# Kernel optimization log

Measured on AMD Instinct MI355X. Metric: run time of the kernel, lower is better.

Reference implementation:

```python
import jax, jax.numpy as jnp
import numpy as np
from jax import lax

HID = 768          # hidden_dim / embedding_dim
IN = 64            # input_dim = max_seq_length // num_heads
SEQ = 512          # max_seq_length
GROUPS = IN        # conv groups
BLUR_K = 5
BLUR_SIGMA = 1.0


def _gauss1d(k, sigma):
    half = (k - 1) * 0.5
    x = np.linspace(-half, half, k)
    pdf = np.exp(-0.5 * (x / sigma) ** 2)
    return pdf / pdf.sum()


def setup_inputs() -> dict:
    key = jax.random.key(0)
    ks = jax.random.split(key, 8)
    s = 0.02
    return {
        "inputs": jax.random.normal(ks[0], (16, SEQ, HID), jnp.float32),
        # Conv1d(768, 768, k=3, groups=64): weight [out_ch, in_ch/groups, k]
        "conv_w": jax.random.normal(ks[1], (HID, HID // GROUPS, 3), jnp.float32) * s,
        "conv_b": jnp.zeros((HID,), jnp.float32),
        "ln_g": jnp.ones((IN,), jnp.float32),
        "ln_b": jnp.zeros((IN,), jnp.float32),
        # function_info: Linear(64, 64), torch weight convention [out, in]
        "fi_w": jax.random.normal(ks[2], (IN, IN), jnp.float32) * s,
        "fi_b": jnp.zeros((IN,), jnp.float32),
        # block_info: Linear(64, 1)
        "bi_w": jax.random.normal(ks[3], (1, IN), jnp.float32) * s,
        "bi_b": jnp.zeros((1,), jnp.float32),
    }


def _forward(inputs, conv_w, conv_b, ln_g, ln_b, fi_w, fi_b, bi_w, bi_b):
    x = inputs.reshape(-1, HID, IN)  # [Bn, 768, 64] (raw row-major view, as torch .view)
    q = k = v = m = x

    # q: grouped Conv1d + residual, GELU, LayerNorm over last dim (64)
    qc = lax.conv_general_dilated(
        q, conv_w, window_strides=(1,), padding=[(1, 1)],
        feature_group_count=GROUPS, dimension_numbers=("NCH", "OIH", "NCH"))
    qc = qc + conv_b[None, :, None]
    q = jax.nn.gelu(qc + q, approximate=False)
    mu = jnp.mean(q, axis=-1, keepdims=True)
    var = jnp.mean(jnp.square(q - mu), axis=-1, keepdims=True)
    q = (q - mu) * lax.rsqrt(var + 1e-5) * ln_g + ln_b

    # v: Linear(64,64) + GELU
    v = jax.nn.gelu(v @ fi_w.T + fi_b, approximate=False)

    # k: dropout (eval -> identity), softmax over dim=-2 (channel axis), GELU
    k = jax.nn.gelu(jax.nn.softmax(k, axis=-2), approximate=False)

    # m: GaussianBlur(5, sigma fixed 1.0) over (H=768, W=64) with reflect pad, then Linear(64,1)
    g = _gauss1d(BLUR_K, BLUR_SIGMA)
    kern = jnp.asarray(np.outer(g, g), m.dtype)[None, None]  # [1,1,5,5]
    p = BLUR_K // 2
    mp = jnp.pad(m[:, None], ((0, 0), (0, 0), (p, p), (p, p)), mode="reflect")
    m = lax.conv_general_dilated(
        mp, kern, (1, 1), "VALID", dimension_numbers=("NCHW", "OIHW", "NCHW"))[:, 0]
    m = m @ bi_w.T + bi_b                        # [Bn, 768, 1]
    mask = jnp.broadcast_to(m, (m.shape[0], HID, HID))  # expand to [Bn,768,768]

    # SDPA: scale = 1/sqrt(E) with E = q.shape[-1] = 64; additive float mask
    scores = jnp.einsum("bce,bde->bcd", q, k) * (1.0 / np.sqrt(IN)) + mask
    attn = jax.nn.softmax(scores, axis=-1)
    out = jnp.einsum("bcd,bde->bce", attn, v)    # [Bn, 768, 64]
    return out.reshape(-1, SEQ, HID)


def reference(inputs, conv_w, conv_b, ln_g, ln_b, fi_w, fi_b, bi_w, bi_b):
    return _forward(inputs, conv_w, conv_b, ln_g, ln_b, fi_w, fi_b, bi_w, bi_b)
```

## Files before the change

kernel.cpp:

```cpp
#include <hip/hip_runtime.h>
#include <hip/hip_bf16.h>
#include <math.h>

#define NB 128
#define NC 768
#define NE 64
#define IPG 12

typedef __hip_bfloat16 bf16;
typedef __bf16 bf16v8 __attribute__((ext_vector_type(8)));
typedef __bf16 bf16v4 __attribute__((ext_vector_type(4)));
typedef __bf16 bf16v2 __attribute__((ext_vector_type(2)));
typedef float f32x4 __attribute__((ext_vector_type(4)));
typedef unsigned int u32;
typedef u32 u32x4 __attribute__((ext_vector_type(4)));

__device__ __forceinline__ float gelu_exact(float x) {
    return 0.5f * x * (1.0f + erff(x * 0.70710678118654752f));
}

#define MFMA16(a, b, c) __builtin_amdgcn_mfma_f32_16x16x32_bf16(a, b, c, 0, 0, 0)

__device__ __forceinline__ void gload_lds16(const void* g, void* l) {
    __builtin_amdgcn_global_load_lds(
        (const __attribute__((address_space(1))) void*)g,
        (__attribute__((address_space(3))) void*)l, 16, 0, 0);
}

__global__ __launch_bounds__(256) void k_stats(const float* __restrict__ x,
                                               float* __restrict__ sp) {
    int part = blockIdx.x, b = blockIdx.y;
    int e = threadIdx.x & 63, sub = threadIdx.x >> 6;
    const float* xb = x + (size_t)b * NC * NE + (size_t)(part * 96 + sub * 24) * NE;
    float s = 0.f;
    #pragma unroll
    for (int c = 0; c < 24; ++c) s += __expf(xb[c * NE + e]);
    __shared__ float red[4][64];
    red[sub][e] = s;
    __syncthreads();
    if (sub == 0)
        sp[(size_t)(b * 8 + part) * 64 + e] =
            red[0][e] + red[1][e] + red[2][e] + red[3][e];
}

__global__ __launch_bounds__(256) void k_conv(
    const float* __restrict__ x, const float* __restrict__ cw,
    const float* __restrict__ cb, const float* __restrict__ lg,
    const float* __restrict__ lb, bf16* __restrict__ qo)
{
    int b = blockIdx.x >> 4;
    int g = (blockIdx.x & 15) * 4 + (threadIdx.x >> 6);
    g = __builtin_amdgcn_readfirstlane(g);
    int h = threadIdx.x & 63;
    const float* xb = x + ((size_t)b * NC + g * IPG) * NE;

    float xi[IPG], xm[IPG], xp[IPG];
    #pragma unroll
    for (int i = 0; i < IPG; ++i) {
        xi[i] = xb[i * NE + h];
        float up = __shfl_up(xi[i], 1);
        float dn = __shfl_down(xi[i], 1);
        xm[i] = h ? up : 0.f;
        xp[i] = (h < 63) ? dn : 0.f;
    }
    float gam = lg[h], bet = lb[h];
    const float* wg = cw + (size_t)g * IPG * 36;

    for (int o = 0; o < IPG; ++o) {
        const float* wo = wg + o * 36;
        float acc = cb[g * IPG + o];
        #pragma unroll
        for (int i = 0; i < IPG; ++i)
            acc = fmaf(xm[i], wo[i*3], fmaf(xi[i], wo[i*3+1], fmaf(xp[i], wo[i*3+2], acc)));
        float gl = gelu_exact(acc + xi[o]);
        float s1 = gl, s2 = gl * gl;
        #pragma unroll
        for (int off = 32; off; off >>= 1) {
            s1 += __shfl_xor(s1, off);
            s2 += __shfl_xor(s2, off);
        }
        float mu  = s1 * (1.f / 64.f);
        float var = s2 * (1.f / 64.f) - mu * mu;
        float qn = (gl - mu) * rsqrtf(var + 1e-5f) * gam + bet;
        qo[((size_t)b * NC + g * IPG + o) * NE + h] = __float2bfloat16(qn * 0.125f);
    }
}

__global__ __launch_bounds__(256) void k_vk(
    const float* __restrict__ x, const float* __restrict__ fw,
    const float* __restrict__ fb, const float* __restrict__ sp,
    bf16* __restrict__ ko, bf16* __restrict__ vTo)
{
    int chunk = blockIdx.x, b = blockIdx.y;
    int tid = threadIdx.x, w = tid >> 6, l = tid & 63;
    int lr = l & 15, lc = (l >> 4) * 8;
    int rowb = chunk * 64 + w * 16;
    const float* xb = x + (size_t)b * NC * NE;

    __shared__ float sts[64];
    if (tid < 64) {
        float s = 0.f;
        #pragma unroll
        for (int p = 0; p < 8; ++p) s += sp[(size_t)(b * 8 + p) * 64 + tid];
        sts[tid] = 1.f / s;
    }

    bf16v8 bfr[4][2];
    float fbias[4];
    #pragma unroll
    for (int nt = 0; nt < 4; ++nt) {
        #pragma unroll
        for (int kt = 0; kt < 2; ++kt) {
            const float* p = fw + (nt*16 + lr) * 64 + kt*32 + lc;
            bf16v8 t;
            #pragma unroll
            for (int j = 0; j < 8; ++j) t[j] = (__bf16)p[j];
            bfr[nt][kt] = t;
        }
        fbias[nt] = fb[nt*16 + lr];
    }
    __syncthreads();

    float isA[8], isB[8];
    #pragma unroll
    for (int j = 0; j < 8; ++j) { isA[j] = sts[lc + j]; isB[j] = sts[32 + lc + j]; }

    const float* pa = xb + (size_t)(rowb + lr) * NE;
    float xa[8], xc[8];
    #pragma unroll
    for (int j = 0; j < 8; ++j) xa[j] = pa[lc + j];
    #pragma unroll
    for (int j = 0; j < 8; ++j) xc[j] = pa[32 + lc + j];

    bf16v8 a0, a1;
    #pragma unroll
    for (int j = 0; j < 8; ++j) a0[j] = (__bf16)xa[j];
    #pragma unroll
    for (int j = 0; j < 8; ++j) a1[j] = (__bf16)xc[j];

    bf16v8 kv0, kv1;
    #pragma unroll
    for (int j = 0; j < 8; ++j) kv0[j] = (__bf16)gelu_exact(__expf(xa[j]) * isA[j]);
    #pragma unroll
    for (int j = 0; j < 8; ++j) kv1[j] = (__bf16)gelu_exact(__expf(xc[j]) * isB[j]);
    bf16* kp = ko + ((size_t)b * NC + rowb + lr) * NE + lc;
    *(bf16v8*)kp = kv0;
    *(bf16v8*)(kp + 32) = kv1;

    #pragma unroll
    for (int nt = 0; nt < 4; ++nt) {
        f32x4 acc = {fbias[nt], fbias[nt], fbias[nt], fbias[nt]};
        acc = MFMA16(a0, bfr[nt][0], acc);
        acc = MFMA16(a1, bfr[nt][1], acc);
        bf16v4 pk;
        #pragma unroll
        for (int r = 0; r < 4; ++r) pk[r] = (__bf16)gelu_exact(acc[r]);
        int c = rowb + (l >> 4) * 4;
        *(bf16v4*)&vTo[((size_t)b * NE + nt*16 + lr) * NC + c] = pk;
    }
}

__device__ __forceinline__ bf16v8 softmax_exch(f32x4 s0, f32x4 s1, float& rsum,
                                               int srcA, int srcB, int hq) {
    float p0 = __expf(s0[0]), p1 = __expf(s0[1]), p2 = __expf(s0[2]), p3 = __expf(s0[3]);
    float p4 = __expf(s1[0]), p5 = __expf(s1[1]), p6 = __expf(s1[2]), p7 = __expf(s1[3]);
    rsum += ((p0 + p1) + (p2 + p3)) + ((p4 + p5) + (p6 + p7));
    bf16v2 t0; t0[0] = (__bf16)p0; t0[1] = (__bf16)p1;
    bf16v2 t1; t1[0] = (__bf16)p2; t1[1] = (__bf16)p3;
    bf16v2 t2; t2[0] = (__bf16)p4; t2[1] = (__bf16)p5;
    bf16v2 t3; t3[0] = (__bf16)p6; t3[1] = (__bf16)p7;
    u32 w0 = __builtin_bit_cast(u32, t0), w1 = __builtin_bit_cast(u32, t1);
    u32 w2 = __builtin_bit_cast(u32, t2), w3 = __builtin_bit_cast(u32, t3);
    u32 c0A = (u32)__shfl((int)w0, srcA), c1A = (u32)__shfl((int)w1, srcA);
    u32 c2A = (u32)__shfl((int)w2, srcA), c3A = (u32)__shfl((int)w3, srcA);
    u32 c0B = (u32)__shfl((int)w0, srcB), c1B = (u32)__shfl((int)w1, srcB);
    u32 c2B = (u32)__shfl((int)w2, srcB), c3B = (u32)__shfl((int)w3, srcB);
    u32x4 pau = { hq ? c2A : c0A, hq ? c3A : c1A,
                  hq ? c2B : c0B, hq ? c3B : c1B };
    return __builtin_bit_cast(bf16v8, pau);
}

__global__ __launch_bounds__(256, 2) void k_attn(const bf16* __restrict__ qb,
                                                 const bf16* __restrict__ kb,
                                                 const bf16* __restrict__ vT,
                                                 float* __restrict__ out) {
    __shared__ __align__(16) __bf16 ldsK[2][4096];
    __shared__ __align__(16) __bf16 ldsV[2][4096];

    int bid = blockIdx.x;
    int swz = (bid & 7) * 96 + (bid >> 3);
    int b = swz / 6, qt = swz - b * 6;
    int w = threadIdx.x >> 6, l = threadIdx.x & 63;
    int q0 = qt * 128 + w * 32;
    int lr = l & 15, hi = l >> 4;
    int hq = hi >> 1;
    int srcA = lr + ((hi & 1) << 5);
    int srcB = srcA + 16;

    int krow_ = w * 8 + (l >> 3);
    int kc16_ = (l & 7) ^ (l >> 3);
    const char* kgbase = (const char*)(kb + (size_t)b * NC * NE)
                       + krow_ * 128 + kc16_ * 16;
    int ve_   = w * 16 + (l >> 2);
    int vc16_ = (l & 3) ^ ((l >> 3) & 3);
    const char* vgbase = (const char*)(vT + (size_t)b * NE * NC)
                       + ve_ * 1536 + vc16_ * 16;

    int krd0 = lr * 64 + ((hi ^ (lr & 7)) << 3);
    int krd1 = lr * 64 + (((4 + hi) ^ (lr & 7)) << 3);
    int vsel = (lr >> 1) & 3;
    int vrd  = lr * 32 + ((hi ^ vsel) << 3);

    const bf16* qp = qb + ((size_t)b * NC + q0 + lr) * NE + hi * 8;
    bf16v8 qf00 = *(const bf16v8*)qp;
    bf16v8 qf01 = *(const bf16v8*)(qp + 32);
    bf16v8 qf10 = *(const bf16v8*)(qp + 16 * NE);
    bf16v8 qf11 = *(const bf16v8*)(qp + 16 * NE + 32);

    f32x4 o00 = {0,0,0,0}, o01 = {0,0,0,0}, o02 = {0,0,0,0}, o03 = {0,0,0,0};
    f32x4 o10 = {0,0,0,0}, o11 = {0,0,0,0}, o12 = {0,0,0,0}, o13 = {0,0,0,0};
    float rsum0 = 0.f, rsum1 = 0.f;

    gload_lds16(kgbase,           &ldsK[0][w * 512]);
    gload_lds16(kgbase + 4096,    &ldsK[0][2048 + w * 512]);
    gload_lds16(vgbase,           &ldsV[0][w * 512]);
    gload_lds16(vgbase + 64,      &ldsV[0][2048 + w * 512]);
    __syncthreads();

    int cur = 0;
    for (int ph = 0; ph < 12; ++ph) {
        if (ph < 11) {
            const char* kg = kgbase + (size_t)(2 * ph + 2) * 4096;
            gload_lds16(kg,        &ldsK[cur ^ 1][w * 512]);
            gload_lds16(kg + 4096, &ldsK[cur ^ 1][2048 + w * 512]);
            const char* vg = vgbase + (size_t)(2 * ph + 2) * 64;
            gload_lds16(vg,        &ldsV[cur ^ 1][w * 512]);
            gload_lds16(vg + 64,   &ldsV[cur ^ 1][2048 + w * 512]);
        }

        #pragma unroll
        for (int sub = 0; sub < 2; ++sub) {
            const __bf16* Kc = &ldsK[cur][sub * 2048];
            const __bf16* Vc = &ldsV[cur][sub * 2048];
            bf16v8 ka0 = *(const bf16v8*)&Kc[krd0];
            bf16v8 ka1 = *(const bf16v8*)&Kc[krd1];
            bf16v8 ka2 = *(const bf16v8*)&Kc[krd0 + 1024];
            bf16v8 ka3 = *(const bf16v8*)&Kc[krd1 + 1024];
            bf16v8 v0  = *(const bf16v8*)&Vc[vrd];
            bf16v8 v1  = *(const bf16v8*)&Vc[vrd + 512];
            bf16v8 v2  = *(const bf16v8*)&Vc[vrd + 1024];
            bf16v8 v3  = *(const bf16v8*)&Vc[vrd + 1536];

            __builtin_amdgcn_s_setprio(1);
            f32x4 s00 = {0,0,0,0}, s01 = {0,0,0,0};
            s00 = MFMA16(ka0, qf00, s00);
            s00 = MFMA16(ka1, qf01, s00);
            s01 = MFMA16(ka2, qf00, s01);
            s01 = MFMA16(ka3, qf01, s01);
            f32x4 s10 = {0,0,0,0}, s11 = {0,0,0,0};
            s10 = MFMA16(ka0, qf10, s10);
            s10 = MFMA16(ka1, qf11, s10);
            s11 = MFMA16(ka2, qf10, s11);
            s11 = MFMA16(ka3, qf11, s11);
            __builtin_amdgcn_s_setprio(0);

            bf16v8 pa0 = softmax_exch(s00, s01, rsum0, srcA, srcB, hq);
            bf16v8 pa1 = softmax_exch(s10, s11, rsum1, srcA, srcB, hq);

            __builtin_amdgcn_s_setprio(1);
            o00 = MFMA16(pa0, v0, o00);
            o01 = MFMA16(pa0, v1, o01);
            o02 = MFMA16(pa0, v2, o02);
            o03 = MFMA16(pa0, v3, o03);
            o10 = MFMA16(pa1, v0, o10);
            o11 = MFMA16(pa1, v1, o11);
            o12 = MFMA16(pa1, v2, o12);
            o13 = MFMA16(pa1, v3, o13);
            __builtin_amdgcn_s_setprio(0);
        }

        __syncthreads();
        cur ^= 1;
    }

    rsum0 += __shfl_xor(rsum0, 16);
    rsum0 += __shfl_xor(rsum0, 32);
    rsum1 += __shfl_xor(rsum1, 16);
    rsum1 += __shfl_xor(rsum1, 32);
    float inv0 = 1.f / rsum0, inv1 = 1.f / rsum1;

    int qrow0 = q0 + hi * 4;
    #pragma unroll
    for (int r = 0; r < 4; ++r) {
        float iq = __shfl(inv0, hi * 4 + r);
        float* op = out + ((size_t)b * NC + qrow0 + r) * NE + lr;
        op[0]  = o00[r] * iq;
        op[16] = o01[r] * iq;
        op[32] = o02[r] * iq;
        op[48] = o03[r] * iq;
    }
    int qrow1 = q0 + 16 + hi * 4;
    #pragma unroll
    for (int r = 0; r < 4; ++r) {
        float iq = __shfl(inv1, hi * 4 + r);
        float* op = out + ((size_t)b * NC + qrow1 + r) * NE + lr;
        op[0]  = o10[r] * iq;
        op[16] = o11[r] * iq;
        op[32] = o12[r] * iq;
        op[48] = o13[r] * iq;
    }
}

extern "C" void kernel_launch(void* const* d_in, const int* in_sizes, int n_in,
                              void* d_out, int out_size, void* d_ws, size_t ws_size,
                              hipStream_t stream) {
    (void)in_sizes; (void)n_in; (void)out_size; (void)ws_size;
    const float* x      = (const float*)d_in[0];
    const float* conv_w = (const float*)d_in[1];
    const float* conv_b = (const float*)d_in[2];
    const float* ln_g   = (const float*)d_in[3];
    const float* ln_b   = (const float*)d_in[4];
    const float* fi_w   = (const float*)d_in[5];
    const float* fi_b   = (const float*)d_in[6];

    bf16* qbuf = (bf16*)d_ws;
    bf16* kbuf = qbuf + (size_t)NB * NC * NE;
    bf16* vT   = kbuf + (size_t)NB * NC * NE;
    float* stats = (float*)(vT + (size_t)NB * NC * NE);
    float* out = (float*)d_out;

    k_stats<<<dim3(8, NB), 256, 0, stream>>>(x, stats);
    k_conv<<<dim3(NB * 16), 256, 0, stream>>>(x, conv_w, conv_b, ln_g, ln_b, qbuf);
    k_vk<<<dim3(12, NB), 256, 0, stream>>>(x, fi_w, fi_b, stats, kbuf, vT);
    k_attn<<<dim3(768), 256, 0, stream>>>(qbuf, kbuf, vT, out);
}
```

Before: 84.71 us.

## Fuse softmax column stats into conv kernel, approximate GELU, raise attn occupancy

Removes the separate k_stats kernel and computes the per-column exp sums inside k_conv from values it already loads, writing 16 partial sums per batch that k_vk then reduces. Replaces erff-based exact GELU with an Abramowitz-Stegun polynomial approximation using a fast reciprocal and exp. Raises the k_attn launch-bounds occupancy hint from 2 to 3 blocks per CU. This saves one kernel launch and one full read of the input, at the cost of GELU accuracy and possible register pressure or spills in k_attn.

```diff
diff --git a/kernel.cpp b/kernel.cpp
--- a/kernel.cpp
+++ b/kernel.cpp
@@ -16,7 +16,14 @@
 typedef u32 u32x4 __attribute__((ext_vector_type(4)));
 
 __device__ __forceinline__ float gelu_exact(float x) {
-    return 0.5f * x * (1.0f + erff(x * 0.70710678118654752f));
+    float ax = fabsf(x);
+    float t = __builtin_amdgcn_rcpf(fmaf(0.2316419f, ax, 1.0f));
+    float poly = t * fmaf(t, fmaf(t, fmaf(t, fmaf(t, 1.330274429f,
+                  -1.821255978f), 1.781477937f), -0.356563782f), 0.319381530f);
+    float pdf = 0.3989422804f * __expf(-0.5f * ax * ax);
+    float c = fmaf(-pdf, poly, 1.0f);
+    float cdf = (x >= 0.f) ? c : 1.0f - c;
+    return x * cdf;
 }
 
 #define MFMA16(a, b, c) __builtin_amdgcn_mfma_f32_16x16x32_bf16(a, b, c, 0, 0, 0)
@@ -27,30 +34,16 @@
         (__attribute__((address_space(3))) void*)l, 16, 0, 0);
 }
 
-__global__ __launch_bounds__(256) void k_stats(const float* __restrict__ x,
-                                               float* __restrict__ sp) {
-    int part = blockIdx.x, b = blockIdx.y;
-    int e = threadIdx.x & 63, sub = threadIdx.x >> 6;
-    const float* xb = x + (size_t)b * NC * NE + (size_t)(part * 96 + sub * 24) * NE;
-    float s = 0.f;
-    #pragma unroll
-    for (int c = 0; c < 24; ++c) s += __expf(xb[c * NE + e]);
-    __shared__ float red[4][64];
-    red[sub][e] = s;
-    __syncthreads();
-    if (sub == 0)
-        sp[(size_t)(b * 8 + part) * 64 + e] =
-            red[0][e] + red[1][e] + red[2][e] + red[3][e];
-}
-
 __global__ __launch_bounds__(256) void k_conv(
     const float* __restrict__ x, const float* __restrict__ cw,
     const float* __restrict__ cb, const float* __restrict__ lg,
-    const float* __restrict__ lb, bf16* __restrict__ qo)
+    const float* __restrict__ lb, bf16* __restrict__ qo,
+    float* __restrict__ sp)
 {
     int b = blockIdx.x >> 4;
-    int g = (blockIdx.x & 15) * 4 + (threadIdx.x >> 6);
-    g = __builtin_amdgcn_readfirstlane(g);
+    int chunk = blockIdx.x & 15;
+    int w = threadIdx.x >> 6;
+    int g = __builtin_amdgcn_readfirstlane(chunk * 4 + w);
     int h = threadIdx.x & 63;
     const float* xb = x + ((size_t)b * NC + g * IPG) * NE;
 
@@ -63,6 +56,18 @@
         xm[i] = h ? up : 0.f;
         xp[i] = (h < 63) ? dn : 0.f;
     }
+
+    float es = 0.f;
+    #pragma unroll
+    for (int i = 0; i < IPG; ++i) es += __expf(xi[i]);
+    __shared__ float red[4][64];
+    red[w][h] = es;
+    __syncthreads();
+    if (w == 0) {
+        float s = red[0][h] + red[1][h] + red[2][h] + red[3][h];
+        sp[(size_t)(b * 16 + chunk) * 64 + h] = s;
+    }
+
     float gam = lg[h], bet = lb[h];
     const float* wg = cw + (size_t)g * IPG * 36;
 
@@ -101,7 +106,7 @@
     if (tid < 64) {
         float s = 0.f;
         #pragma unroll
-        for (int p = 0; p < 8; ++p) s += sp[(size_t)(b * 8 + p) * 64 + tid];
+        for (int p = 0; p < 16; ++p) s += sp[(size_t)(b * 16 + p) * 64 + tid];
         sts[tid] = 1.f / s;
     }
 
@@ -180,7 +185,7 @@
     return __builtin_bit_cast(bf16v8, pau);
 }
 
-__global__ __launch_bounds__(256, 2) void k_attn(const bf16* __restrict__ qb,
+__global__ __launch_bounds__(256, 3) void k_attn(const bf16* __restrict__ qb,
                                                  const bf16* __restrict__ kb,
                                                  const bf16* __restrict__ vT,
                                                  float* __restrict__ out) {
@@ -329,8 +334,8 @@
     float* stats = (float*)(vT + (size_t)NB * NC * NE);
     float* out = (float*)d_out;
 
-    k_stats<<<dim3(8, NB), 256, 0, stream>>>(x, stats);
-    k_conv<<<dim3(NB * 16), 256, 0, stream>>>(x, conv_w, conv_b, ln_g, ln_b, qbuf);
+    k_conv<<<dim3(NB * 16), 256, 0, stream>>>(x, conv_w, conv_b, ln_g, ln_b,
+                                              qbuf, stats);
     k_vk<<<dim3(12, NB), 256, 0, stream>>>(x, fi_w, fi_b, stats, kbuf, vT);
     k_attn<<<dim3(768), 256, 0, stream>>>(qbuf, kbuf, vT, out);
 }
```

Measured after the change: 78.89 us. 1.07x faster.
